# Performance work log

Hardware: AMD Instinct MI355X
Metric: run time of the kernel (lower is better)

The kernel has to match this reference:

```python
import jax, jax.numpy as jnp
import numpy as np
from jax import lax

NPOINT = 1024
RADIUS = 0.4
NSAMPLE = 32
EPS = 1e-5


def setup_inputs() -> dict:
    key = jax.random.key(0)
    ks = jax.random.split(key, 8)
    B, N, Cin = 16, 4096, 64
    mlp = [64, 64, 128]
    last = Cin + 3
    inp = {
        "xyz": jax.random.normal(ks[0], (B, N, 3), dtype=jnp.float32),
        "points": jax.random.normal(ks[1], (B, N, Cin), dtype=jnp.float32),
    }
    for i, co in enumerate(mlp):
        inp[f"w{i}"] = jax.random.normal(ks[2 + i], (co, last), dtype=jnp.float32) * 0.05
        inp[f"b{i}"] = jnp.zeros((co,), jnp.float32)
        inp[f"g{i}"] = jnp.ones((co,), jnp.float32)
        inp[f"be{i}"] = jnp.zeros((co,), jnp.float32)
        last = co
    return inp


def _gather(pts, idx):
    # pts: [B, N, C], idx: [B, ...] -> [B, ..., C]
    return jax.vmap(lambda p, i: p[i])(pts, idx)


def farthest_point_sample(xyz, npoint):
    # Deterministic variant: start from index 0 (torch uses a random start).
    B, N, _ = xyz.shape
    bidx = jnp.arange(B)

    def step(carry, _):
        distance, farthest = carry
        centroid = xyz[bidx, farthest][:, None, :]          # [B,1,3]
        dist = jnp.sum((xyz - centroid) ** 2, -1)           # [B,N]
        distance = jnp.minimum(distance, dist)
        return (distance, jnp.argmax(distance, -1)), farthest

    init = (jnp.full((B, N), 1e10, xyz.dtype), jnp.zeros((B,), jnp.int32))
    _, cent = lax.scan(step, init, None, length=npoint)
    return cent.T                                            # [B, npoint]


def query_ball_point(radius, nsample, xyz, new_xyz):
    B, N, _ = xyz.shape
    # [B, S, N] squared distances centroid -> all points
    sqr = jnp.sum((xyz[:, None, :, :] - new_xyz[:, :, None, :]) ** 2, -1)
    gi = jnp.where(sqr > radius ** 2, N, jnp.arange(N)[None, None, :])
    gi = jnp.sort(gi, axis=-1)[:, :, :nsample]               # smallest in-ball indices
    gi = jnp.where(gi == N, gi[:, :, :1], gi)                # pad with first neighbor
    return gi


def reference(xyz, points, w0, b0, g0, be0, w1, b1, g1, be1, w2, b2, g2, be2):
    B, N, _ = xyz.shape
    cent = farthest_point_sample(xyz, NPOINT)                # [B,S]
    new_xyz = _gather(xyz, cent)                             # [B,S,3]
    gi = query_ball_point(RADIUS, NSAMPLE, xyz, new_xyz)     # [B,S,K]
    grouped_xyz = _gather(xyz, gi) - new_xyz[:, :, None, :]  # [B,S,K,3]
    x = jnp.concatenate([grouped_xyz, _gather(points, gi)], -1)  # [B,S,K,3+Cin]
    for w, b, g, be in ((w0, b0, g0, be0), (w1, b1, g1, be1), (w2, b2, g2, be2)):
        x = jnp.einsum('bskc,oc->bsko', x, w) + b            # 1x1 conv
        m = jnp.mean(x, axis=(0, 1, 2))
        v = jnp.var(x, axis=(0, 1, 2))                       # biased var, as torch BN
        x = jax.nn.relu(g * (x - m) * lax.rsqrt(v + EPS) + be)
    new_points = jnp.max(x, axis=2)                          # max over nsample -> [B,S,Cout]
    return new_xyz, new_points
```

## Files before the change

kernel.cpp:

```cpp
#include <hip/hip_runtime.h>
#include <hip/hip_bf16.h>
#include <math.h>


static constexpr int BATCH  = 16;
static constexpr int NPTS   = 4096;
static constexpr int NPOINT = 1024;
static constexpr int NSAMP  = 32;
static constexpr int CIN    = 64;
static constexpr int ROWS   = BATCH * NPOINT * NSAMP;
static constexpr int NBLK   = ROWS / 64;

typedef unsigned long long u64;
typedef float f32x4 __attribute__((ext_vector_type(4)));
typedef short short8v __attribute__((ext_vector_type(8)));

__device__ __forceinline__ float sqdist(float x, float y, float z,
                                        float cx, float cy, float cz) {
    float dx = x - cx, dy = y - cy, dz = z - cz;
    return __fadd_rn(__fadd_rn(__fmul_rn(dx, dx), __fmul_rn(dy, dy)), __fmul_rn(dz, dz));
}

#if __has_builtin(__builtin_amdgcn_update_dpp) && __has_builtin(__builtin_amdgcn_readlane)
#define DPP_FMAX(x, ctrl)                                                             \
    do {                                                                              \
        int _o = __builtin_amdgcn_update_dpp(__float_as_int(x), __float_as_int(x),    \
                                             (ctrl), 0xf, 0xf, false);                \
        (x) = fmaxf((x), __int_as_float(_o));                                         \
    } while (0)
#define WAVE_RED_F(x) do { DPP_FMAX(x,0x111); DPP_FMAX(x,0x112); DPP_FMAX(x,0x114); \
                           DPP_FMAX(x,0x118); DPP_FMAX(x,0x142); DPP_FMAX(x,0x143); } while (0)
__device__ __forceinline__ float bcast63(float v) {
    return __int_as_float(__builtin_amdgcn_readlane(__float_as_int(v), 63));
}
#else
#define WAVE_RED_F(x) do { for (int _m = 1; _m < 64; _m <<= 1) (x) = fmaxf((x), __shfl_xor((x), _m)); } while (0)
__device__ __forceinline__ float bcast63(float v) { return __shfl(v, 63); }
#endif

__device__ __forceinline__ unsigned short f2bf(float v) {
    union { __hip_bfloat16 b; unsigned short u; } c;
    c.b = __float2bfloat16(v);
    return c.u;
}

__device__ __forceinline__ int swz(int row, int bir) {
    return (row << 7) | (bir ^ ((row & 7) << 4));
}

__device__ __forceinline__ short8v load_frag(const char* b, int row, int k0) {
    union { uint2 v; short s[4]; } lo, hi;
    lo.v = *(const uint2*)(b + swz(row, 2 * k0));
    hi.v = *(const uint2*)(b + swz(row, 2 * k0 + 32));
    short8v f;
    f[0] = lo.s[0]; f[1] = lo.s[1]; f[2] = lo.s[2]; f[3] = lo.s[3];
    f[4] = hi.s[0]; f[5] = hi.s[1]; f[6] = hi.s[2]; f[7] = hi.s[3];
    return f;
}

__global__ __launch_bounds__(512) void pre_kernel(
    const float* __restrict__ xyz, const float* __restrict__ points,
    const float* __restrict__ w0, const float* __restrict__ b0,
    float* __restrict__ P, float* __restrict__ new_xyz) {
    __shared__ __align__(16) char s_raw[53376];
    const int tid = threadIdx.x;

    if (blockIdx.x < 16) {
        float2* sxy    = (float2*)s_raw;
        float*  szv    = (float*)(s_raw + 32768);
        int*    s_cent = (int*)(s_raw + 49152);
        u64*    s_red  = (u64*)(s_raw + 53248);

        const int b = blockIdx.x;
        const float* xb = xyz + (size_t)b * NPTS * 3;
        for (int p = tid; p < NPTS; p += 512) {
            sxy[p] = make_float2(xb[p * 3 + 0], xb[p * 3 + 1]);
            szv[p] = xb[p * 3 + 2];
        }
        __syncthreads();
        float px[8], py[8], pz[8], dist[8];
#pragma unroll
        for (int j = 0; j < 8; ++j) {
            int p = tid + j * 512;
            float2 f = sxy[p];
            px[j] = f.x; py[j] = f.y; pz[j] = szv[p];
            dist[j] = 1e10f;
        }
        const int lane = tid & 63, wid = tid >> 6;
        int far = 0;
        for (int it = 0; it < NPOINT; ++it) {
            if (tid == 0) s_cent[it] = far;
            const float2 cxy = sxy[far];
            const float  cz  = szv[far];
            float bv = -1.0f;
            int   bi = 0;
#pragma unroll
            for (int j = 0; j < 8; ++j) {
                float d  = sqdist(px[j], py[j], pz[j], cxy.x, cxy.y, cz);
                float nd = fminf(dist[j], d);
                dist[j]  = nd;
                if (nd > bv) { bv = nd; bi = tid + j * 512; }
            }
            float gmax = bv;
            WAVE_RED_F(gmax);
            gmax = bcast63(gmax);
            u64 mask = __ballot(bv == gmax);
            int widx = __shfl(bi, (int)__builtin_ctzll(mask));
            if (lane == 0)
                s_red[(it & 1) * 8 + wid] =
                    ((u64)__float_as_uint(gmax) << 32) | (unsigned)(4095 - widx);
            __syncthreads();
            const u64* sr = &s_red[(it & 1) * 8];
            u64 w = sr[0];
#pragma unroll
            for (int k = 1; k < 8; ++k) { u64 o = sr[k]; w = (o > w) ? o : w; }
            far = 4095 - (int)(w & 0xffffffffu);
        }
        __syncthreads();
        for (int s = tid; s < NPOINT; s += 512) {
            int c = s_cent[s];
            float2 f = sxy[c];
            new_xyz[((size_t)b * NPOINT + s) * 3 + 0] = f.x;
            new_xyz[((size_t)b * NPOINT + s) * 3 + 1] = f.y;
            new_xyz[((size_t)b * NPOINT + s) * 3 + 2] = szv[c];
        }
    } else {
        float (*xw)[68] = (float(*)[68])s_raw;
        float (*wt)[68] = (float(*)[68])(s_raw + 34816);
        const int blk = blockIdx.x - 16;
        const int pt0 = blk * 128;
        const int ty = tid >> 4, tx = tid & 15;

        for (int idx = tid; idx < 128 * 3; idx += 512) {
            int r = idx / 3, d = idx - r * 3;
            xw[r][d] = xyz[(size_t)(pt0 + r) * 3 + d];
        }
        for (int idx = tid; idx < 128 * 16; idx += 512) {
            int r = idx >> 4, c4 = idx & 15;
            float4 v = *(const float4*)(points + (size_t)(pt0 + r) * CIN + c4 * 4);
            xw[r][3 + c4 * 4 + 0] = v.x;
            xw[r][3 + c4 * 4 + 1] = v.y;
            xw[r][3 + c4 * 4 + 2] = v.z;
            xw[r][3 + c4 * 4 + 3] = v.w;
        }
        for (int idx = tid; idx < 64 * 67; idx += 512) {
            int o = idx / 67, c = idx - o * 67;
            wt[o][c] = w0[idx];
        }
        __syncthreads();

        float acc[4][4];
        {
            float bj[4];
#pragma unroll
            for (int j = 0; j < 4; ++j) bj[j] = b0[tx + 16 * j];
#pragma unroll
            for (int i = 0; i < 4; ++i)
#pragma unroll
                for (int j = 0; j < 4; ++j) acc[i][j] = bj[j];
        }
        for (int c4 = 0; c4 < 64; c4 += 4) {
            float4 xv[4], wv[4];
#pragma unroll
            for (int i = 0; i < 4; ++i) xv[i] = *(const float4*)&xw[ty + 32 * i][c4];
#pragma unroll
            for (int j = 0; j < 4; ++j) wv[j] = *(const float4*)&wt[tx + 16 * j][c4];
#pragma unroll
            for (int i = 0; i < 4; ++i)
#pragma unroll
                for (int j = 0; j < 4; ++j)
                    acc[i][j] += xv[i].x * wv[j].x + xv[i].y * wv[j].y +
                                 xv[i].z * wv[j].z + xv[i].w * wv[j].w;
        }
#pragma unroll
        for (int c = 64; c < 67; ++c) {
            float xv[4], wv[4];
#pragma unroll
            for (int i = 0; i < 4; ++i) xv[i] = xw[ty + 32 * i][c];
#pragma unroll
            for (int j = 0; j < 4; ++j) wv[j] = wt[tx + 16 * j][c];
#pragma unroll
            for (int i = 0; i < 4; ++i)
#pragma unroll
                for (int j = 0; j < 4; ++j) acc[i][j] += xv[i] * wv[j];
        }
#pragma unroll
        for (int i = 0; i < 4; ++i)
#pragma unroll
            for (int j = 0; j < 4; ++j)
                P[(size_t)(pt0 + ty + 32 * i) * 64 + tx + 16 * j] = acc[i][j];
    }
}

__global__ __launch_bounds__(256) void ballq_kernel(const float* __restrict__ xyz,
                                                    const float* __restrict__ new_xyz,
                                                    const float* __restrict__ w0,
                                                    int* __restrict__ gi,
                                                    float* __restrict__ Q) {
    const int lane = threadIdx.x & 63;
    const int w    = threadIdx.x >> 6;
    const int pair = blockIdx.x * 4 + w;
    const int b    = pair >> 10;
    const float R2 = (float)(0.4 * 0.4);
    const float* xb = xyz + (size_t)b * NPTS * 3;
    const float cx = new_xyz[pair * 3 + 0];
    const float cy = new_xyz[pair * 3 + 1];
    const float cz = new_xyz[pair * 3 + 2];
    int* g = gi + (size_t)pair * NSAMP;

    Q[(size_t)pair * 64 + lane] =
        w0[lane * 67 + 0] * cx + w0[lane * 67 + 1] * cy + w0[lane * 67 + 2] * cz;

    int found = 0, first = 0;
    bool have_first = false;
    for (int c0 = 0; c0 < NPTS; c0 += 64) {
        const int n = c0 + lane;
        float d = sqdist(xb[n * 3 + 0], xb[n * 3 + 1], xb[n * 3 + 2], cx, cy, cz);
        bool in = !(d > R2);
        unsigned long long m = __ballot(in);
        if (m) {
            if (!have_first) { first = c0 + (__ffsll(m) - 1); have_first = true; }
            if (in) {
                int slot = found + (int)__popcll(m & ((1ull << lane) - 1ull));
                if (slot < NSAMP) g[slot] = n;
            }
            found += (int)__popcll(m);
            if (found >= NSAMP) break;
        }
    }
    for (int slot = found + lane; slot < NSAMP; slot += 64) g[slot] = first;
}

__global__ __launch_bounds__(256) void stats0_kernel(
    const float* __restrict__ P, const float* __restrict__ Q,
    const int* __restrict__ gi, float* __restrict__ partial) {
    __shared__ __align__(16) float xw[64][68];
    __shared__ int s_n[64];
    const int tid = threadIdx.x, blk = blockIdx.x;
    const int row0 = blk * 64;
    if (tid < 64) s_n[tid] = ((row0 + tid) >> 15) * NPTS + gi[row0 + tid];
    __syncthreads();
    for (int idx = tid; idx < 64 * 16; idx += 256) {
        int r = idx >> 4, c4 = idx & 15;
        float4 pv = *(const float4*)(P + ((size_t)s_n[r] << 6) + c4 * 4);
        float4 qv = *(const float4*)(Q + ((size_t)(blk * 2 + (r >> 5)) << 6) + c4 * 4);
        float4 y; y.x = pv.x - qv.x; y.y = pv.y - qv.y; y.z = pv.z - qv.z; y.w = pv.w - qv.w;
        *(float4*)&xw[r][c4 * 4] = y;
    }
    __syncthreads();
    if (tid < 64) {
        float s = 0.f, q = 0.f;
        for (int r = 0; r < 64; ++r) { float v = xw[r][tid]; s += v; q += v * v; }
        partial[(size_t)blk * 128 + tid]      = s;
        partial[(size_t)blk * 128 + 64 + tid] = q;
    }
}

__global__ __launch_bounds__(256) void chainM1_kernel(
    const float* __restrict__ P, const float* __restrict__ Q,
    const int* __restrict__ gi, const float* __restrict__ w1, const float* __restrict__ b1,
    const float* __restrict__ ss, float* __restrict__ partial) {
    __shared__ __align__(16) char h0b[64 * 128];
    __shared__ __align__(16) char w1b[64 * 128];
    __shared__ float sredS[4][64], sredQ[4][64];
    __shared__ int s_n[64];
    const int tid = threadIdx.x, blk = blockIdx.x;
    const int row0 = blk * 64;
    if (tid < 64) s_n[tid] = ((row0 + tid) >> 15) * NPTS + gi[row0 + tid];
    for (int idx = tid; idx < 1024; idx += 256) {
        float4 v = *(const float4*)(w1 + idx * 4);
        uint2 pk; pk.x = (unsigned)f2bf(v.x) | ((unsigned)f2bf(v.y) << 16);
        pk.y = (unsigned)f2bf(v.z) | ((unsigned)f2bf(v.w) << 16);
        *(uint2*)(w1b + swz(idx >> 4, 8 * (idx & 15))) = pk;
    }
    __syncthreads();
    for (int idx = tid; idx < 1024; idx += 256) {
        int r = idx >> 4, c0 = (idx & 15) * 4;
        float4 pv = *(const float4*)(P + ((size_t)s_n[r] << 6) + c0);
        float4 qv = *(const float4*)(Q + ((size_t)(blk * 2 + (r >> 5)) << 6) + c0);
        float4 sc = *(const float4*)(ss + c0);
        float4 sh = *(const float4*)(ss + 128 + c0);
        float y0 = fmaxf((pv.x - qv.x) * sc.x + sh.x, 0.f);
        float y1v = fmaxf((pv.y - qv.y) * sc.y + sh.y, 0.f);
        float y2v = fmaxf((pv.z - qv.z) * sc.z + sh.z, 0.f);
        float y3 = fmaxf((pv.w - qv.w) * sc.w + sh.w, 0.f);
        uint2 pk; pk.x = (unsigned)f2bf(y0) | ((unsigned)f2bf(y1v) << 16);
        pk.y = (unsigned)f2bf(y2v) | ((unsigned)f2bf(y3) << 16);
        *(uint2*)(h0b + swz(r, 8 * (idx & 15))) = pk;
    }
    __syncthreads();

    const int l = tid & 63, w = tid >> 6;
    const int mrow = 16 * w + (l & 15);
    const int klane = (l >> 4) * 4;
    short8v a0 = load_frag(h0b, mrow, klane);
    short8v a1 = load_frag(h0b, mrow, klane + 32);
#pragma unroll
    for (int nt = 0; nt < 4; ++nt) {
        float bias = b1[16 * nt + (l & 15)];
        f32x4 acc; acc[0] = bias; acc[1] = bias; acc[2] = bias; acc[3] = bias;
        short8v bA = load_frag(w1b, 16 * nt + (l & 15), klane);
        short8v bB = load_frag(w1b, 16 * nt + (l & 15), klane + 32);
        acc = __builtin_amdgcn_mfma_f32_16x16x32_bf16(a0, bA, acc, 0, 0, 0);
        acc = __builtin_amdgcn_mfma_f32_16x16x32_bf16(a1, bB, acc, 0, 0, 0);
        float s = acc[0] + acc[1] + acc[2] + acc[3];
        float q = acc[0] * acc[0] + acc[1] * acc[1] + acc[2] * acc[2] + acc[3] * acc[3];
        s += __shfl_xor(s, 16); s += __shfl_xor(s, 32);
        q += __shfl_xor(q, 16); q += __shfl_xor(q, 32);
        if (l < 16) { sredS[w][nt * 16 + l] = s; sredQ[w][nt * 16 + l] = q; }
    }
    __syncthreads();
    if (tid < 64) {
        float s = sredS[0][tid] + sredS[1][tid] + sredS[2][tid] + sredS[3][tid];
        float q = sredQ[0][tid] + sredQ[1][tid] + sredQ[2][tid] + sredQ[3][tid];
        partial[(size_t)blk * 128 + tid]      = s;
        partial[(size_t)blk * 128 + 64 + tid] = q;
    }
}

__global__ __launch_bounds__(256) void chainM2_kernel(
    const float* __restrict__ P, const float* __restrict__ Q,
    const int* __restrict__ gi,
    const float* __restrict__ w1, const float* __restrict__ b1,
    const float* __restrict__ w2, const float* __restrict__ b2,
    const float* __restrict__ ss, float* __restrict__ partial,
    float* __restrict__ maxy) {
    __shared__ __align__(16) char h0b[64 * 128];
    __shared__ __align__(16) char w1b[64 * 128];
    __shared__ __align__(16) char h1b[64 * 128];
    __shared__ __align__(16) char w2b[128 * 128];
    __shared__ float sredS[4][128], sredQ[4][128], sredM[4][128];
    __shared__ int s_n[64];
    const int tid = threadIdx.x, blk = blockIdx.x;
    const int row0 = blk * 64;
    if (tid < 64) s_n[tid] = ((row0 + tid) >> 15) * NPTS + gi[row0 + tid];
    for (int idx = tid; idx < 1024; idx += 256) {
        float4 v = *(const float4*)(w1 + idx * 4);
        uint2 pk; pk.x = (unsigned)f2bf(v.x) | ((unsigned)f2bf(v.y) << 16);
        pk.y = (unsigned)f2bf(v.z) | ((unsigned)f2bf(v.w) << 16);
        *(uint2*)(w1b + swz(idx >> 4, 8 * (idx & 15))) = pk;
    }
    for (int idx = tid; idx < 2048; idx += 256) {
        float4 v = *(const float4*)(w2 + idx * 4);
        uint2 pk; pk.x = (unsigned)f2bf(v.x) | ((unsigned)f2bf(v.y) << 16);
        pk.y = (unsigned)f2bf(v.z) | ((unsigned)f2bf(v.w) << 16);
        *(uint2*)(w2b + swz(idx >> 4, 8 * (idx & 15))) = pk;
    }
    __syncthreads();
    for (int idx = tid; idx < 1024; idx += 256) {
        int r = idx >> 4, c0 = (idx & 15) * 4;
        float4 pv = *(const float4*)(P + ((size_t)s_n[r] << 6) + c0);
        float4 qv = *(const float4*)(Q + ((size_t)(blk * 2 + (r >> 5)) << 6) + c0);
        float4 sc = *(const float4*)(ss + c0);
        float4 sh = *(const float4*)(ss + 128 + c0);
        float y0 = fmaxf((pv.x - qv.x) * sc.x + sh.x, 0.f);
        float y1v = fmaxf((pv.y - qv.y) * sc.y + sh.y, 0.f);
        float y2v = fmaxf((pv.z - qv.z) * sc.z + sh.z, 0.f);
        float y3 = fmaxf((pv.w - qv.w) * sc.w + sh.w, 0.f);
        uint2 pk; pk.x = (unsigned)f2bf(y0) | ((unsigned)f2bf(y1v) << 16);
        pk.y = (unsigned)f2bf(y2v) | ((unsigned)f2bf(y3) << 16);
        *(uint2*)(h0b + swz(r, 8 * (idx & 15))) = pk;
    }
    __syncthreads();

    const int l = tid & 63, w = tid >> 6;
    const int mrow = 16 * w + (l & 15);
    const int klane = (l >> 4) * 4;
    {
        short8v a0 = load_frag(h0b, mrow, klane);
        short8v a1 = load_frag(h0b, mrow, klane + 32);
#pragma unroll
        for (int nt = 0; nt < 4; ++nt) {
            float bias = b1[16 * nt + (l & 15)];
            f32x4 acc; acc[0] = bias; acc[1] = bias; acc[2] = bias; acc[3] = bias;
            short8v bA = load_frag(w1b, 16 * nt + (l & 15), klane);
            short8v bB = load_frag(w1b, 16 * nt + (l & 15), klane + 32);
            acc = __builtin_amdgcn_mfma_f32_16x16x32_bf16(a0, bA, acc, 0, 0, 0);
            acc = __builtin_amdgcn_mfma_f32_16x16x32_bf16(a1, bB, acc, 0, 0, 0);
#pragma unroll
            for (int p = 0; p < 4; ++p) {
                int row = 16 * w + (l >> 4) * 4 + p;
                int col = 16 * nt + (l & 15);
                float v = fmaxf(acc[p] * ss[256 + col] + ss[384 + col], 0.f);
                *(unsigned short*)(h1b + swz(row, 2 * col)) = f2bf(v);
            }
        }
    }
    __syncthreads();
    {
        short8v a0 = load_frag(h1b, mrow, klane);
        short8v a1 = load_frag(h1b, mrow, klane + 32);
#pragma unroll
        for (int nt = 0; nt < 8; ++nt) {
            float bias = b2[16 * nt + (l & 15)];
            f32x4 acc; acc[0] = bias; acc[1] = bias; acc[2] = bias; acc[3] = bias;
            short8v bA = load_frag(w2b, 16 * nt + (l & 15), klane);
            short8v bB = load_frag(w2b, 16 * nt + (l & 15), klane + 32);
            acc = __builtin_amdgcn_mfma_f32_16x16x32_bf16(a0, bA, acc, 0, 0, 0);
            acc = __builtin_amdgcn_mfma_f32_16x16x32_bf16(a1, bB, acc, 0, 0, 0);
            float s = acc[0] + acc[1] + acc[2] + acc[3];
            float q = acc[0] * acc[0] + acc[1] * acc[1] + acc[2] * acc[2] + acc[3] * acc[3];
            float m = fmaxf(fmaxf(acc[0], acc[1]), fmaxf(acc[2], acc[3]));
            s += __shfl_xor(s, 16); s += __shfl_xor(s, 32);
            q += __shfl_xor(q, 16); q += __shfl_xor(q, 32);
            m = fmaxf(m, __shfl_xor(m, 16)); m = fmaxf(m, __shfl_xor(m, 32));
            if (l < 16) {
                sredS[w][nt * 16 + l] = s;
                sredQ[w][nt * 16 + l] = q;
                sredM[w][nt * 16 + l] = m;
            }
        }
    }
    __syncthreads();
    if (tid < 128) {
        float s = sredS[0][tid] + sredS[1][tid] + sredS[2][tid] + sredS[3][tid];
        float q = sredQ[0][tid] + sredQ[1][tid] + sredQ[2][tid] + sredQ[3][tid];
        partial[(size_t)blk * 256 + tid]       = s;
        partial[(size_t)blk * 256 + 128 + tid] = q;
        const int bs0 = blk * 2;
        maxy[(size_t)bs0 * 128 + tid]       = fmaxf(sredM[0][tid], sredM[1][tid]);
        maxy[(size_t)(bs0 + 1) * 128 + tid] = fmaxf(sredM[2][tid], sredM[3][tid]);
    }
}

__global__ __launch_bounds__(256) void reduce_stats_kernel(
    const float* __restrict__ partial, int Cd, float inv_count,
    const float* __restrict__ g, const float* __restrict__ be,
    float* __restrict__ ss_layer) {
    const int c   = blockIdx.x;
    const int tid = threadIdx.x;
    float s = 0.f, q = 0.f;
    for (int blk = tid; blk < NBLK; blk += 256) {
        s += partial[(size_t)blk * 2 * Cd + c];
        q += partial[(size_t)blk * 2 * Cd + Cd + c];
    }
#pragma unroll
    for (int m = 1; m < 64; m <<= 1) { s += __shfl_xor(s, m); q += __shfl_xor(q, m); }
    __shared__ float ls[4], lq[4];
    const int wid = tid >> 6;
    if ((tid & 63) == 0) { ls[wid] = s; lq[wid] = q; }
    __syncthreads();
    if (tid == 0) {
        s = ls[0] + ls[1] + ls[2] + ls[3];
        q = lq[0] + lq[1] + lq[2] + lq[3];
        float mean = s * inv_count;
        float var  = q * inv_count - mean * mean;
        float sc   = g[c] / sqrtf(var + 1e-5f);
        ss_layer[c]       = sc;
        ss_layer[128 + c] = be[c] - mean * sc;
    }
}

__global__ __launch_bounds__(256) void final_kernel(const float* __restrict__ maxy,
                                                    const float* __restrict__ ss2,
                                                    float* __restrict__ outp) {
    int idx = blockIdx.x * 256 + threadIdx.x;
    int c = idx & 127;
    float v = maxy[idx] * ss2[c] + ss2[128 + c];
    outp[idx] = fmaxf(v, 0.f);
}

extern "C" void kernel_launch(void* const* d_in, const int* in_sizes, int n_in,
                              void* d_out, int out_size, void* d_ws, size_t ws_size,
                              hipStream_t stream) {
    const float* xyz    = (const float*)d_in[0];
    const float* points = (const float*)d_in[1];
    const float* w0 = (const float*)d_in[2];  const float* b0  = (const float*)d_in[3];
    const float* g0 = (const float*)d_in[4];  const float* be0 = (const float*)d_in[5];
    const float* w1 = (const float*)d_in[6];  const float* b1  = (const float*)d_in[7];
    const float* g1 = (const float*)d_in[8];  const float* be1 = (const float*)d_in[9];
    const float* w2 = (const float*)d_in[10]; const float* b2  = (const float*)d_in[11];
    const float* g2 = (const float*)d_in[12]; const float* be2 = (const float*)d_in[13];

    float* out      = (float*)d_out;
    float* new_xyz  = out;
    float* out_pts  = out + (size_t)BATCH * NPOINT * 3;

    char* p = (char*)d_ws;
    int* gi = (int*)p;          p += (((size_t)ROWS * 4) + 255) & ~(size_t)255;
    float* partial = (float*)p; p += (((size_t)NBLK * 256 * 4) + 255) & ~(size_t)255;
    float* ss = (float*)p;      p += ((size_t)(3 * 256 * 4) + 255) & ~(size_t)255;
    float* maxy = (float*)p;    p += (((size_t)BATCH * NPOINT * 128 * 4) + 255) & ~(size_t)255;
    float* P = (float*)p;       p += (((size_t)BATCH * NPTS * 64 * 4) + 255) & ~(size_t)255;
    float* Q = (float*)p;

    const float inv_count = 1.0f / (float)ROWS;

    pre_kernel<<<16 + 512, 512, 0, stream>>>(xyz, points, w0, b0, P, new_xyz);
    ballq_kernel<<<(BATCH * NPOINT) / 4, 256, 0, stream>>>(xyz, new_xyz, w0, gi, Q);

    stats0_kernel<<<NBLK, 256, 0, stream>>>(P, Q, gi, partial);
    reduce_stats_kernel<<<64, 256, 0, stream>>>(partial, 64, inv_count, g0, be0, ss + 0);

    chainM1_kernel<<<NBLK, 256, 0, stream>>>(P, Q, gi, w1, b1, ss, partial);
    reduce_stats_kernel<<<64, 256, 0, stream>>>(partial, 64, inv_count, g1, be1, ss + 256);

    chainM2_kernel<<<NBLK, 256, 0, stream>>>(P, Q, gi, w1, b1, w2, b2, ss, partial, maxy);
    reduce_stats_kernel<<<128, 256, 0, stream>>>(partial, 128, inv_count, g2, be2, ss + 512);

    final_kernel<<<(BATCH * NPOINT * 128) / 256, 256, 0, stream>>>(maxy, ss + 512, out_pts);
}
```

Measured before the change: 908.1 us.

## Fuse layer-0 BN statistics into ball query kernel and drop stats0 launch

The ball-query kernel now keeps each centroid's 32 neighbor indices in shared memory. It then gathers P rows directly to accumulate per-pair channel sums and sums of squares, which removes the separate stats0 kernel and its reread of gi. The reduce kernel takes a variable block count, since layer 0 now has NPAIR partials, twice the previous count, so the reduction reads twice as much. The FPS argmax also writes the winning index from the owning lane instead of using a shuffle.

```diff
diff --git a/kernel.cpp b/kernel.cpp
--- a/kernel.cpp
+++ b/kernel.cpp
@@ -10,6 +10,7 @@
 static constexpr int CIN    = 64;
 static constexpr int ROWS   = BATCH * NPOINT * NSAMP;
 static constexpr int NBLK   = ROWS / 64;
+static constexpr int NPAIR  = BATCH * NPOINT;
 
 typedef unsigned long long u64;
 typedef float f32x4 __attribute__((ext_vector_type(4)));
@@ -105,10 +106,9 @@
             WAVE_RED_F(gmax);
             gmax = bcast63(gmax);
             u64 mask = __ballot(bv == gmax);
-            int widx = __shfl(bi, (int)__builtin_ctzll(mask));
-            if (lane == 0)
+            if (bv == gmax && lane == (int)__builtin_ctzll(mask))
                 s_red[(it & 1) * 8 + wid] =
-                    ((u64)__float_as_uint(gmax) << 32) | (unsigned)(4095 - widx);
+                    ((u64)__float_as_uint(gmax) << 32) | (unsigned)(4095 - bi);
             __syncthreads();
             const u64* sr = &s_red[(it & 1) * 8];
             u64 w = sr[0];
@@ -195,8 +195,11 @@
 __global__ __launch_bounds__(256) void ballq_kernel(const float* __restrict__ xyz,
                                                     const float* __restrict__ new_xyz,
                                                     const float* __restrict__ w0,
+                                                    const float* __restrict__ P,
                                                     int* __restrict__ gi,
-                                                    float* __restrict__ Q) {
+                                                    float* __restrict__ Q,
+                                                    float* __restrict__ partial) {
+    __shared__ int sn[4][32];
     const int lane = threadIdx.x & 63;
     const int w    = threadIdx.x >> 6;
     const int pair = blockIdx.x * 4 + w;
@@ -208,8 +211,9 @@
     const float cz = new_xyz[pair * 3 + 2];
     int* g = gi + (size_t)pair * NSAMP;
 
-    Q[(size_t)pair * 64 + lane] =
+    const float qv =
         w0[lane * 67 + 0] * cx + w0[lane * 67 + 1] * cy + w0[lane * 67 + 2] * cz;
+    Q[(size_t)pair * 64 + lane] = qv;
 
     int found = 0, first = 0;
     bool have_first = false;
@@ -222,38 +226,25 @@
             if (!have_first) { first = c0 + (__ffsll(m) - 1); have_first = true; }
             if (in) {
                 int slot = found + (int)__popcll(m & ((1ull << lane) - 1ull));
-                if (slot < NSAMP) g[slot] = n;
+                if (slot < NSAMP) { g[slot] = n; sn[w][slot] = n; }
             }
             found += (int)__popcll(m);
             if (found >= NSAMP) break;
         }
     }
-    for (int slot = found + lane; slot < NSAMP; slot += 64) g[slot] = first;
-}
-
-__global__ __launch_bounds__(256) void stats0_kernel(
-    const float* __restrict__ P, const float* __restrict__ Q,
-    const int* __restrict__ gi, float* __restrict__ partial) {
-    __shared__ __align__(16) float xw[64][68];
-    __shared__ int s_n[64];
-    const int tid = threadIdx.x, blk = blockIdx.x;
-    const int row0 = blk * 64;
-    if (tid < 64) s_n[tid] = ((row0 + tid) >> 15) * NPTS + gi[row0 + tid];
-    __syncthreads();
-    for (int idx = tid; idx < 64 * 16; idx += 256) {
-        int r = idx >> 4, c4 = idx & 15;
-        float4 pv = *(const float4*)(P + ((size_t)s_n[r] << 6) + c4 * 4);
-        float4 qv = *(const float4*)(Q + ((size_t)(blk * 2 + (r >> 5)) << 6) + c4 * 4);
-        float4 y; y.x = pv.x - qv.x; y.y = pv.y - qv.y; y.z = pv.z - qv.z; y.w = pv.w - qv.w;
-        *(float4*)&xw[r][c4 * 4] = y;
-    }
-    __syncthreads();
-    if (tid < 64) {
-        float s = 0.f, q = 0.f;
-        for (int r = 0; r < 64; ++r) { float v = xw[r][tid]; s += v; q += v * v; }
-        partial[(size_t)blk * 128 + tid]      = s;
-        partial[(size_t)blk * 128 + 64 + tid] = q;
-    }
+    for (int slot = found + lane; slot < NSAMP; slot += 64) { g[slot] = first; sn[w][slot] = first; }
+    __syncthreads();
+
+    const float* Pb = P + (((size_t)b * NPTS) << 6);
+    float s = 0.f, q = 0.f;
+#pragma unroll 8
+    for (int k = 0; k < NSAMP; ++k) {
+        float pv = Pb[((size_t)sn[w][k] << 6) + lane];
+        float y = pv - qv;
+        s += y; q += y * y;
+    }
+    partial[(size_t)pair * 128 + lane]      = s;
+    partial[(size_t)pair * 128 + 64 + lane] = q;
 }
 
 __global__ __launch_bounds__(256) void chainM1_kernel(
@@ -424,13 +415,13 @@
 }
 
 __global__ __launch_bounds__(256) void reduce_stats_kernel(
-    const float* __restrict__ partial, int Cd, float inv_count,
+    const float* __restrict__ partial, int Cd, int nblk, float inv_count,
     const float* __restrict__ g, const float* __restrict__ be,
     float* __restrict__ ss_layer) {
     const int c   = blockIdx.x;
     const int tid = threadIdx.x;
     float s = 0.f, q = 0.f;
-    for (int blk = tid; blk < NBLK; blk += 256) {
+    for (int blk = tid; blk < nblk; blk += 256) {
         s += partial[(size_t)blk * 2 * Cd + c];
         q += partial[(size_t)blk * 2 * Cd + Cd + c];
     }
@@ -478,7 +469,7 @@
 
     char* p = (char*)d_ws;
     int* gi = (int*)p;          p += (((size_t)ROWS * 4) + 255) & ~(size_t)255;
-    float* partial = (float*)p; p += (((size_t)NBLK * 256 * 4) + 255) & ~(size_t)255;
+    float* partial = (float*)p; p += (((size_t)NPAIR * 128 * 4) + 255) & ~(size_t)255;
     float* ss = (float*)p;      p += ((size_t)(3 * 256 * 4) + 255) & ~(size_t)255;
     float* maxy = (float*)p;    p += (((size_t)BATCH * NPOINT * 128 * 4) + 255) & ~(size_t)255;
     float* P = (float*)p;       p += (((size_t)BATCH * NPTS * 64 * 4) + 255) & ~(size_t)255;
@@ -487,16 +478,14 @@
     const float inv_count = 1.0f / (float)ROWS;
 
     pre_kernel<<<16 + 512, 512, 0, stream>>>(xyz, points, w0, b0, P, new_xyz);
-    ballq_kernel<<<(BATCH * NPOINT) / 4, 256, 0, stream>>>(xyz, new_xyz, w0, gi, Q);
-
-    stats0_kernel<<<NBLK, 256, 0, stream>>>(P, Q, gi, partial);
-    reduce_stats_kernel<<<64, 256, 0, stream>>>(partial, 64, inv_count, g0, be0, ss + 0);
+    ballq_kernel<<<NPAIR / 4, 256, 0, stream>>>(xyz, new_xyz, w0, P, gi, Q, partial);
+    reduce_stats_kernel<<<64, 256, 0, stream>>>(partial, 64, NPAIR, inv_count, g0, be0, ss + 0);
 
     chainM1_kernel<<<NBLK, 256, 0, stream>>>(P, Q, gi, w1, b1, ss, partial);
-    reduce_stats_kernel<<<64, 256, 0, stream>>>(partial, 64, inv_count, g1, be1, ss + 256);
+    reduce_stats_kernel<<<64, 256, 0, stream>>>(partial, 64, NBLK, inv_count, g1, be1, ss + 256);
 
     chainM2_kernel<<<NBLK, 256, 0, stream>>>(P, Q, gi, w1, b1, w2, b2, ss, partial, maxy);
-    reduce_stats_kernel<<<128, 256, 0, stream>>>(partial, 128, inv_count, g2, be2, ss + 512);
+    reduce_stats_kernel<<<128, 256, 0, stream>>>(partial, 128, NBLK, inv_count, g2, be2, ss + 512);
 
     final_kernel<<<(BATCH * NPOINT * 128) / 256, 256, 0, stream>>>(maxy, ss + 512, out_pts);
 }
```

Result: slower. 946.8 us (+4.3%).
